# Kernel optimization log

Hardware: AMD Instinct MI355X
Metric: run time of the kernel (lower is better)

The kernel has to match this reference:

```python
import jax, jax.numpy as jnp
import numpy as np

N_NODES = 100000
N_EDGES = 1600000
IN_CH, HID_CH, OUT_CH = 128, 256, 128


def _sage_conv(x, src, dst, W_l, b_l, W_r, n_nodes):
    """PyG SAGEConv with mean aggregation: lin_l(mean_j x_j) + lin_r(x)."""
    # gather source features per edge, scatter-sum into destination nodes
    agg = jax.ops.segment_sum(x[src], dst, num_segments=n_nodes)  # [N, C]
    deg = jax.ops.segment_sum(jnp.ones((src.shape[0],), x.dtype), dst,
                              num_segments=n_nodes)               # [N]
    mean = agg / jnp.maximum(deg, 1.0)[:, None]
    return mean @ W_l + b_l + x @ W_r


def setup_inputs() -> dict:
    key = jax.random.key(0)
    ks = jax.random.split(key, 8)
    x = jax.random.normal(ks[0], (N_NODES, IN_CH), dtype=jnp.float32)
    edge_index = jax.random.randint(ks[1], (2, N_EDGES), 0, N_NODES, dtype=jnp.int64)
    s1 = 1.0 / np.sqrt(IN_CH)
    s2 = 1.0 / np.sqrt(HID_CH)
    W1_l = jax.random.normal(ks[2], (IN_CH, HID_CH), dtype=jnp.float32) * s1
    W1_r = jax.random.normal(ks[3], (IN_CH, HID_CH), dtype=jnp.float32) * s1
    b1 = jnp.zeros((HID_CH,), dtype=jnp.float32)
    W2_l = jax.random.normal(ks[4], (HID_CH, OUT_CH), dtype=jnp.float32) * s2
    W2_r = jax.random.normal(ks[5], (HID_CH, OUT_CH), dtype=jnp.float32) * s2
    b2 = jnp.zeros((OUT_CH,), dtype=jnp.float32)
    return {"x": x, "edge_index": edge_index, "W1_l": W1_l, "b1": b1,
            "W1_r": W1_r, "W2_l": W2_l, "b2": b2, "W2_r": W2_r}


def reference(x, edge_index, W1_l, b1, W1_r, W2_l, b2, W2_r):
    src, dst = edge_index[0], edge_index[1]
    h = _sage_conv(x, src, dst, W1_l, b1, W1_r, N_NODES)
    h = jax.nn.relu(h)
    out = _sage_conv(h, src, dst, W2_l, b2, W2_r, N_NODES)
    return out
```

## Files before the change

kernel.cpp:

```cpp
#include <hip/hip_runtime.h>
#include <cstddef>

#define N_NODES_C 100000
#define N_EDGES_C 1600000

#define NPB 63
#define NB 1588
#define DIV_MAGIC 68174085ULL
#define BCAP 1408
#define SENT_ROW 100000

#define CONV_BLOCKS 12500
#define WB_BLOCKS 512
#define P1_BLOCKS 1563

typedef unsigned short u16;
typedef __attribute__((ext_vector_type(8))) short bf16x8;
typedef __attribute__((ext_vector_type(4))) float f32x4;

__device__ __forceinline__ u16 f2bf(float f) {
    unsigned u = __float_as_uint(f);
    u += 0x7fffu + ((u >> 16) & 1);
    return (u16)(u >> 16);
}
__device__ __forceinline__ float lo16f(unsigned v) {
    return __uint_as_float(v << 16);
}
__device__ __forceinline__ float hi16f(unsigned v) {
    return __uint_as_float(v & 0xffff0000u);
}
__device__ __forceinline__ unsigned bucket_of(int d) {
    return (unsigned)(((unsigned long long)(unsigned)d * DIV_MAGIC) >> 32);
}


__global__ __launch_bounds__(256) void front_fused(
    const float* __restrict__ x, const int* __restrict__ dst,
    const float* __restrict__ W1l, const float* __restrict__ W1r,
    const float* __restrict__ W2l, const float* __restrict__ W2r,
    u16* __restrict__ x_bf, u16* __restrict__ T1l, u16* __restrict__ T1r,
    u16* __restrict__ T2l, u16* __restrict__ T2r,
    int* __restrict__ bucket_counts, u16* __restrict__ p2z) {
    const int b = blockIdx.x;
    const int t = threadIdx.x;
    if (b < CONV_BLOCKS) {
        int i = b * 256 + t;
        if (i < 3200000) {
            float4 v = ((const float4*)x)[i];
            ushort4 o;
            o.x = f2bf(v.x); o.y = f2bf(v.y); o.z = f2bf(v.z); o.w = f2bf(v.w);
            ((ushort4*)x_bf)[i] = o;
        }
    } else if (b < CONV_BLOCKS + WB_BLOCKS) {
        int id = (b - CONV_BLOCKS) * 256 + t;
        int which = id >> 15;
        int r = id & 32767;
        if (which == 0) {
            int n = r >> 7, k = r & 127;
            T1l[r] = f2bf(W1l[k * 256 + n]);
        } else if (which == 1) {
            int n = r >> 7, k = r & 127;
            T1r[r] = f2bf(W1r[k * 256 + n]);
        } else if (which == 2) {
            int n = r >> 8, k = r & 255;
            T2l[r] = f2bf(W2l[k * 128 + n]);
        } else {
            int n = r >> 8, k = r & 255;
            T2r[r] = f2bf(W2r[k * 128 + n]);
        }
    } else if (b < CONV_BLOCKS + WB_BLOCKS + P1_BLOCKS) {
        __shared__ int hist[NB];
        for (int j = t; j < NB; j += 256) hist[j] = 0;
        __syncthreads();
        int i = (b - CONV_BLOCKS - WB_BLOCKS) * 256 + t;
        if (i * 4 < N_EDGES_C) {
            int4 d = ((const int4*)dst)[i];
            atomicAdd(&hist[bucket_of(d.x)], 1);
            atomicAdd(&hist[bucket_of(d.y)], 1);
            atomicAdd(&hist[bucket_of(d.z)], 1);
            atomicAdd(&hist[bucket_of(d.w)], 1);
        }
        __syncthreads();
        for (int j = t; j < NB; j += 256) {
            int c = hist[j];
            if (c) atomicAdd(&bucket_counts[j], c);
        }
    } else {
        uint4 z; z.x = 0; z.y = 0; z.z = 0; z.w = 0;
        if (t < 16)
            ((uint4*)(x_bf + (size_t)SENT_ROW * 128))[t] = z;
        else if (t < 32)
            ((uint4*)(p2z + (size_t)SENT_ROW * 128))[t - 16] = z;
    }
}


__global__ __launch_bounds__(1024) void bucket_scan(const int* __restrict__ counts,
                                                    int* __restrict__ base,
                                                    int* __restrict__ cursor) {
    __shared__ int s[1024];
    int t = threadIdx.x;
    int c0 = counts[2 * t];
    int c1 = counts[2 * t + 1];
    int v = c0 + c1;
    s[t] = v;
    __syncthreads();
    for (int off = 1; off < 1024; off <<= 1) {
        int u = (t >= off) ? s[t - off] : 0;
        __syncthreads();
        s[t] += u;
        __syncthreads();
    }
    int excl = s[t] - v;
    base[2 * t] = excl;
    cursor[2 * t] = excl;
    base[2 * t + 1] = excl + c0;
    cursor[2 * t + 1] = excl + c0;
}


__global__ __launch_bounds__(1024) void p2_scatter(const int* __restrict__ src,
                                                   const int* __restrict__ dst,
                                                   int* __restrict__ cursor,
                                                   unsigned* __restrict__ edge_pkt) {
    __shared__ int hist[NB];
    __shared__ int lbase[NB];
    __shared__ int cur2[NB];
    int t = threadIdx.x;
    for (int j = t; j < NB; j += 1024) { hist[j] = 0; cur2[j] = 0; }
    __syncthreads();

    int4 dd[4];
    int idx[4];
#pragma unroll
    for (int r = 0; r < 4; ++r) {
        int i = blockIdx.x * 4096 + r * 1024 + t;
        idx[r] = i;
        if (i * 4 < N_EDGES_C) {
            int4 d = ((const int4*)dst)[i];
            dd[r] = d;
            atomicAdd(&hist[bucket_of(d.x)], 1);
            atomicAdd(&hist[bucket_of(d.y)], 1);
            atomicAdd(&hist[bucket_of(d.z)], 1);
            atomicAdd(&hist[bucket_of(d.w)], 1);
        }
    }
    __syncthreads();
    for (int j = t; j < NB; j += 1024) {
        int c = hist[j];
        if (c) lbase[j] = atomicAdd(&cursor[j], c);
    }
    __syncthreads();

#pragma unroll
    for (int r = 0; r < 4; ++r) {
        int i = idx[r];
        if (i * 4 < N_EDGES_C) {
            int4 s4 = ((const int4*)src)[i];
            int4 d = dd[r];
            {
                unsigned b = bucket_of(d.x);
                int local = d.x - (int)b * NPB;
                int pos = lbase[b] + atomicAdd(&cur2[b], 1);
                edge_pkt[pos] = ((unsigned)local << 17) | (unsigned)s4.x;
            }
            {
                unsigned b = bucket_of(d.y);
                int local = d.y - (int)b * NPB;
                int pos = lbase[b] + atomicAdd(&cur2[b], 1);
                edge_pkt[pos] = ((unsigned)local << 17) | (unsigned)s4.y;
            }
            {
                unsigned b = bucket_of(d.z);
                int local = d.z - (int)b * NPB;
                int pos = lbase[b] + atomicAdd(&cur2[b], 1);
                edge_pkt[pos] = ((unsigned)local << 17) | (unsigned)s4.z;
            }
            {
                unsigned b = bucket_of(d.w);
                int local = d.w - (int)b * NPB;
                int pos = lbase[b] + atomicAdd(&cur2[b], 1);
                edge_pkt[pos] = ((unsigned)local << 17) | (unsigned)s4.w;
            }
        }
    }
}


template <bool FINAL>
__global__ __launch_bounds__(256, 8) void agg_bucket(const u16* __restrict__ tbl,
                                                     const int* __restrict__ base,
                                                     const unsigned* __restrict__ edge_pkt,
                                                     const u16* __restrict__ resid,
                                                     void* __restrict__ outv) {
    __shared__ unsigned se[BCAP];
    __shared__ int lhist[64];
    __shared__ int lstart[64];
    __shared__ int lcur[64];
    __shared__ int stmp[64];

    const int t = threadIdx.x;
    const int wave = t >> 6;
    const int lane = t & 63;
    const int b = blockIdx.x;

    if (t < 64) lhist[t] = 0;
    __syncthreads();

    const int ebeg = base[b];
    int ecnt = base[b + 1] - ebeg;
    if (ecnt > BCAP) ecnt = BCAP;

    for (int i = t; i < ecnt; i += 256)
        atomicAdd(&lhist[edge_pkt[ebeg + i] >> 17], 1);
    __syncthreads();

    if (t < 64) stmp[t] = lhist[t];
    __syncthreads();
    for (int off = 1; off < 64; off <<= 1) {
        int v = 0;
        if (t < 64 && t >= off) v = stmp[t - off];
        __syncthreads();
        if (t < 64) stmp[t] += v;
        __syncthreads();
    }
    if (t < 64) {
        int excl = stmp[t] - lhist[t];
        lstart[t] = excl;
        lcur[t] = excl;
    }
    __syncthreads();

    for (int i = t; i < ecnt; i += 256) {
        unsigned p = edge_pkt[ebeg + i];
        int pos = atomicAdd(&lcur[p >> 17], 1);
        se[pos] = p & 0x1ffffu;
    }
    __syncthreads();

    const int g = lane >> 4;
    const int li8 = (lane & 15) * 8;

    for (int pass = 0; pass < 4; ++pass) {
        int n = pass * 16 + wave * 4 + g;
        int node = b * NPB + n;
        int d = 0, s0 = 0;
        bool valid = (n < NPB) && (node < N_NODES_C);
        if (valid) { d = lhist[n]; s0 = lstart[n]; }
        int dmax = max(d, __shfl_xor(d, 16, 64));
        dmax = max(dmax, __shfl_xor(dmax, 32, 64));

        float a0 = 0.f, a1 = 0.f, a2 = 0.f, a3 = 0.f;
        float a4 = 0.f, a5 = 0.f, a6 = 0.f, a7 = 0.f;

        for (int j = 0; j < dmax; j += 4) {
            unsigned ix[4];
#pragma unroll
            for (int u = 0; u < 4; ++u) {
                int jj = j + u;
                int sa = s0 + jj;
                if (sa > BCAP - 1) sa = BCAP - 1;
                unsigned sv = se[sa];
                ix[u] = (jj < d) ? sv : (unsigned)SENT_ROW;
            }
            uint4 r0 = *(const uint4*)(tbl + (size_t)ix[0] * 128 + li8);
            uint4 r1 = *(const uint4*)(tbl + (size_t)ix[1] * 128 + li8);
            uint4 r2 = *(const uint4*)(tbl + (size_t)ix[2] * 128 + li8);
            uint4 r3 = *(const uint4*)(tbl + (size_t)ix[3] * 128 + li8);

            a0 += lo16f(r0.x); a1 += hi16f(r0.x);
            a2 += lo16f(r0.y); a3 += hi16f(r0.y);
            a4 += lo16f(r0.z); a5 += hi16f(r0.z);
            a6 += lo16f(r0.w); a7 += hi16f(r0.w);
            a0 += lo16f(r1.x); a1 += hi16f(r1.x);
            a2 += lo16f(r1.y); a3 += hi16f(r1.y);
            a4 += lo16f(r1.z); a5 += hi16f(r1.z);
            a6 += lo16f(r1.w); a7 += hi16f(r1.w);
            a0 += lo16f(r2.x); a1 += hi16f(r2.x);
            a2 += lo16f(r2.y); a3 += hi16f(r2.y);
            a4 += lo16f(r2.z); a5 += hi16f(r2.z);
            a6 += lo16f(r2.w); a7 += hi16f(r2.w);
            a0 += lo16f(r3.x); a1 += hi16f(r3.x);
            a2 += lo16f(r3.y); a3 += hi16f(r3.y);
            a4 += lo16f(r3.z); a5 += hi16f(r3.z);
            a6 += lo16f(r3.w); a7 += hi16f(r3.w);
        }

        if (valid) {
            float inv = d > 0 ? 1.f / (float)d : 0.f;
            if (FINAL) {
                uint4 rp = *(const uint4*)(resid + (size_t)node * 128 + li8);
                float* op = (float*)outv + (size_t)node * 128 + li8;
                float4 o0, o1;
                o0.x = a0 * inv + lo16f(rp.x);
                o0.y = a1 * inv + hi16f(rp.x);
                o0.z = a2 * inv + lo16f(rp.y);
                o0.w = a3 * inv + hi16f(rp.y);
                o1.x = a4 * inv + lo16f(rp.z);
                o1.y = a5 * inv + hi16f(rp.z);
                o1.z = a6 * inv + lo16f(rp.w);
                o1.w = a7 * inv + hi16f(rp.w);
                *(float4*)op = o0;
                *(float4*)(op + 4) = o1;
            } else {
                uint4 o;
                o.x = (unsigned)f2bf(a0 * inv) | ((unsigned)f2bf(a1 * inv) << 16);
                o.y = (unsigned)f2bf(a2 * inv) | ((unsigned)f2bf(a3 * inv) << 16);
                o.z = (unsigned)f2bf(a4 * inv) | ((unsigned)f2bf(a5 * inv) << 16);
                o.w = (unsigned)f2bf(a6 * inv) | ((unsigned)f2bf(a7 * inv) << 16);
                *(uint4*)((u16*)outv + (size_t)node * 128 + li8) = o;
            }
        }
    }
}


__global__ __launch_bounds__(256) void fused_l1l2(
    const u16* __restrict__ A1 , const u16* __restrict__ A2 ,
    const u16* __restrict__ T1l, const u16* __restrict__ T1r,
    const u16* __restrict__ T2l, const u16* __restrict__ T2r,
    const float* __restrict__ b1, const float* __restrict__ b2,
    u16* __restrict__ p2, u16* __restrict__ outp, int M) {
    alignas(16) __shared__ u16 hfrag[64 * 256];
    alignas(16) __shared__ u16 As[64 * 32];
    alignas(16) __shared__ u16 Bs[256 * 32];

    const int tid = threadIdx.x;
    const int lane = tid & 63;
    const int wave = tid >> 6;
    const int qm = lane & 15;
    const int quad = lane >> 4;
    const int m0 = blockIdx.x * 64;

    const int wr0 = (wave >> 1) * 32;
    const int wc0 = (wave & 1) * 128;
    f32x4 acch[2][8];
#pragma unroll
    for (int i = 0; i < 2; ++i)
#pragma unroll
        for (int j = 0; j < 8; ++j) acch[i][j] = (f32x4){0.f, 0.f, 0.f, 0.f};

#pragma unroll
    for (int mat = 0; mat < 2; ++mat) {
        const u16* __restrict__ A = mat ? A2 : A1;
        const u16* __restrict__ W = mat ? T1r : T1l;
#pragma unroll
        for (int k0 = 0; k0 < 128; k0 += 32) {
            {
                int c = tid;
                int row = c >> 2, kc = c & 3;
                __builtin_amdgcn_global_load_lds(
                    (const __attribute__((address_space(1))) unsigned*)(
                        A + (size_t)(m0 + row) * 128 + k0 + kc * 8),
                    (__attribute__((address_space(3))) unsigned*)(As + c * 8), 16, 0, 0);
            }
#pragma unroll
            for (int r = 0; r < 4; ++r) {
                int c = r * 256 + tid;
                int row = c >> 2, kc = c & 3;
                __builtin_amdgcn_global_load_lds(
                    (const __attribute__((address_space(1))) unsigned*)(
                        W + (size_t)row * 128 + k0 + kc * 8),
                    (__attribute__((address_space(3))) unsigned*)(Bs + c * 8), 16, 0, 0);
            }
            __syncthreads();
            bf16x8 af[2], bf[8];
#pragma unroll
            for (int i = 0; i < 2; ++i)
                af[i] = *(const bf16x8*)(As + (wr0 + i * 16 + qm) * 32 + quad * 8);
#pragma unroll
            for (int j = 0; j < 8; ++j)
                bf[j] = *(const bf16x8*)(Bs + (wc0 + j * 16 + qm) * 32 + quad * 8);
#pragma unroll
            for (int i = 0; i < 2; ++i)
#pragma unroll
                for (int j = 0; j < 8; ++j)
                    acch[i][j] = __builtin_amdgcn_mfma_f32_16x16x32_bf16(
                        af[i], bf[j], acch[i][j], 0, 0, 0);
            __syncthreads();
        }
    }

#pragma unroll
    for (int j = 0; j < 8; ++j) {
        int n = wc0 + j * 16 + qm;
        float bb = b1[n];
        int ks = n >> 5, quadB = (n >> 3) & 3, jB = n & 7;
#pragma unroll
        for (int i = 0; i < 2; ++i) {
#pragma unroll
            for (int r = 0; r < 4; ++r) {
                int mloc = wr0 + i * 16 + quad * 4 + r;
                float v = fmaxf(acch[i][j][r] + bb, 0.f);
                hfrag[((ks * 4 + (mloc >> 4)) * 16 + (mloc & 15)) * 32 + quadB * 8 + jB] =
                    f2bf(v);
            }
        }
    }
    __syncthreads();

    const int wrB = (wave >> 1) * 32;
    const int wcB = (wave & 1) * 64;
    f32x4 accp[2][4], acco[2][4];
#pragma unroll
    for (int i = 0; i < 2; ++i)
#pragma unroll
        for (int j = 0; j < 4; ++j) {
            accp[i][j] = (f32x4){0.f, 0.f, 0.f, 0.f};
            acco[i][j] = (f32x4){0.f, 0.f, 0.f, 0.f};
        }

#pragma unroll
    for (int ks = 0; ks < 8; ++ks) {
#pragma unroll
        for (int r = 0; r < 4; ++r) {
            int c = r * 256 + tid;
            int matc = c >> 9;
            int row = (c >> 2) & 127;
            int kc = c & 3;
            const u16* W = matc ? T2r : T2l;
            __builtin_amdgcn_global_load_lds(
                (const __attribute__((address_space(1))) unsigned*)(
                    W + (size_t)row * 256 + ks * 32 + kc * 8),
                (__attribute__((address_space(3))) unsigned*)(Bs + c * 8), 16, 0, 0);
        }
        __syncthreads();
        bf16x8 af[2], bfl[4], bfr[4];
#pragma unroll
        for (int i = 0; i < 2; ++i)
            af[i] = *(const bf16x8*)(hfrag +
                                     ((ks * 4 + (wrB >> 4) + i) * 16 + qm) * 32 + quad * 8);
#pragma unroll
        for (int j = 0; j < 4; ++j) {
            bfl[j] = *(const bf16x8*)(Bs + (wcB + j * 16 + qm) * 32 + quad * 8);
            bfr[j] = *(const bf16x8*)(Bs + 4096 + (wcB + j * 16 + qm) * 32 + quad * 8);
        }
#pragma unroll
        for (int i = 0; i < 2; ++i)
#pragma unroll
            for (int j = 0; j < 4; ++j) {
                accp[i][j] = __builtin_amdgcn_mfma_f32_16x16x32_bf16(af[i], bfl[j],
                                                                    accp[i][j], 0, 0, 0);
                acco[i][j] = __builtin_amdgcn_mfma_f32_16x16x32_bf16(af[i], bfr[j],
                                                                    acco[i][j], 0, 0, 0);
            }
        __syncthreads();
    }

#pragma unroll
    for (int j = 0; j < 4; ++j) {
        int n = wcB + j * 16 + qm;
        float bb2 = b2[n];
#pragma unroll
        for (int i = 0; i < 2; ++i) {
#pragma unroll
            for (int r = 0; r < 4; ++r) {
                int row = m0 + wrB + i * 16 + quad * 4 + r;
                if (row < M) {
                    p2[(size_t)row * 128 + n] = f2bf(accp[i][j][r]);
                    outp[(size_t)row * 128 + n] = f2bf(acco[i][j][r] + bb2);
                }
            }
        }
    }
}


extern "C" void kernel_launch(void* const* d_in, const int* in_sizes, int n_in,
                              void* d_out, int out_size, void* d_ws, size_t ws_size,
                              hipStream_t stream) {
    const float* x = (const float*)d_in[0];
    const int* ei = (const int*)d_in[1];
    const float* W1l = (const float*)d_in[2];
    const float* b1 = (const float*)d_in[3];
    const float* W1r = (const float*)d_in[4];
    const float* W2l = (const float*)d_in[5];
    const float* b2 = (const float*)d_in[6];
    const float* W2r = (const float*)d_in[7];
    float* out = (float*)d_out;

    const int* src = ei;
    const int* dst = ei + N_EDGES_C;

    int* iw = (int*)d_ws;
    int* bucket_counts = iw;
    int* bucket_base = iw + 2048;
    int* cursor = iw + 4096;
    unsigned* edge_pkt = (unsigned*)(iw + 6144);
    u16* T1l = (u16*)(iw + 1606144);
    u16* T1r = T1l + 32768;
    u16* T2l = T1r + 32768;
    u16* T2r = T2l + 32768;
    u16* ub = (u16*)((char*)d_ws + (8u << 20));
    u16* x_bf = ub;
    u16* mean1 = ub + 12850000;
    u16* p2 = ub + 25700000;
    u16* outp = ub + 38550000;

    hipMemsetAsync(bucket_counts, 0, 2048 * sizeof(int), stream);

    front_fused<<<CONV_BLOCKS + WB_BLOCKS + P1_BLOCKS + 1, 256, 0, stream>>>(
        x, dst, W1l, W1r, W2l, W2r, x_bf, T1l, T1r, T2l, T2r, bucket_counts, p2);
    bucket_scan<<<1, 1024, 0, stream>>>(bucket_counts, bucket_base, cursor);
    p2_scatter<<<(N_EDGES_C / 4 + 4095) / 4096, 1024, 0, stream>>>(src, dst, cursor,
                                                                   edge_pkt);

    agg_bucket<false><<<NB, 256, 0, stream>>>(x_bf, bucket_base, edge_pkt, nullptr,
                                              mean1);
    fused_l1l2<<<(N_NODES_C + 63) / 64, 256, 0, stream>>>(
        mean1, x_bf, T1l, T1r, T2l, T2r, b1, b2, p2, outp, N_NODES_C);
    agg_bucket<true><<<NB, 256, 0, stream>>>(p2, bucket_base, edge_pkt, outp, out);
}
```

Before: 401.9 us.

## Fuse layer-1 aggregation into GEMM kernel with 64-node power-of-two buckets

```diff
diff --git a/kernel.cpp b/kernel.cpp
--- a/kernel.cpp
+++ b/kernel.cpp
@@ -4,9 +4,8 @@
 #define N_NODES_C 100000
 #define N_EDGES_C 1600000
 
-#define NPB 63
-#define NB 1588
-#define DIV_MAGIC 68174085ULL
+#define NPB 64
+#define NB 1563
 #define BCAP 1408
 #define SENT_ROW 100000
 
@@ -28,9 +27,6 @@
 }
 __device__ __forceinline__ float hi16f(unsigned v) {
     return __uint_as_float(v & 0xffff0000u);
-}
-__device__ __forceinline__ unsigned bucket_of(int d) {
-    return (unsigned)(((unsigned long long)(unsigned)d * DIV_MAGIC) >> 32);
 }
 
 
@@ -75,10 +71,10 @@
         int i = (b - CONV_BLOCKS - WB_BLOCKS) * 256 + t;
         if (i * 4 < N_EDGES_C) {
             int4 d = ((const int4*)dst)[i];
-            atomicAdd(&hist[bucket_of(d.x)], 1);
-            atomicAdd(&hist[bucket_of(d.y)], 1);
-            atomicAdd(&hist[bucket_of(d.z)], 1);
-            atomicAdd(&hist[bucket_of(d.w)], 1);
+            atomicAdd(&hist[d.x >> 6], 1);
+            atomicAdd(&hist[d.y >> 6], 1);
+            atomicAdd(&hist[d.z >> 6], 1);
+            atomicAdd(&hist[d.w >> 6], 1);
         }
         __syncthreads();
         for (int j = t; j < NB; j += 256) {
@@ -139,10 +135,10 @@
         if (i * 4 < N_EDGES_C) {
             int4 d = ((const int4*)dst)[i];
             dd[r] = d;
-            atomicAdd(&hist[bucket_of(d.x)], 1);
-            atomicAdd(&hist[bucket_of(d.y)], 1);
-            atomicAdd(&hist[bucket_of(d.z)], 1);
-            atomicAdd(&hist[bucket_of(d.w)], 1);
+            atomicAdd(&hist[d.x >> 6], 1);
+            atomicAdd(&hist[d.y >> 6], 1);
+            atomicAdd(&hist[d.z >> 6], 1);
+            atomicAdd(&hist[d.w >> 6], 1);
         }
     }
     __syncthreads();
@@ -159,27 +155,23 @@
             int4 s4 = ((const int4*)src)[i];
             int4 d = dd[r];
             {
-                unsigned b = bucket_of(d.x);
-                int local = d.x - (int)b * NPB;
-                int pos = lbase[b] + atomicAdd(&cur2[b], 1);
+                int bk = d.x >> 6, local = d.x & 63;
+                int pos = lbase[bk] + atomicAdd(&cur2[bk], 1);
                 edge_pkt[pos] = ((unsigned)local << 17) | (unsigned)s4.x;
             }
             {
-                unsigned b = bucket_of(d.y);
-                int local = d.y - (int)b * NPB;
-                int pos = lbase[b] + atomicAdd(&cur2[b], 1);
+                int bk = d.y >> 6, local = d.y & 63;
+                int pos = lbase[bk] + atomicAdd(&cur2[bk], 1);
                 edge_pkt[pos] = ((unsigned)local << 17) | (unsigned)s4.y;
             }
             {
-                unsigned b = bucket_of(d.z);
-                int local = d.z - (int)b * NPB;
-                int pos = lbase[b] + atomicAdd(&cur2[b], 1);
+                int bk = d.z >> 6, local = d.z & 63;
+                int pos = lbase[bk] + atomicAdd(&cur2[bk], 1);
                 edge_pkt[pos] = ((unsigned)local << 17) | (unsigned)s4.z;
             }
             {
-                unsigned b = bucket_of(d.w);
-                int local = d.w - (int)b * NPB;
-                int pos = lbase[b] + atomicAdd(&cur2[b], 1);
+                int bk = d.w >> 6, local = d.w & 63;
+                int pos = lbase[bk] + atomicAdd(&cur2[bk], 1);
                 edge_pkt[pos] = ((unsigned)local << 17) | (unsigned)s4.w;
             }
         }
@@ -187,66 +179,85 @@
 }
 
 
-template <bool FINAL>
-__global__ __launch_bounds__(256, 8) void agg_bucket(const u16* __restrict__ tbl,
-                                                     const int* __restrict__ base,
-                                                     const unsigned* __restrict__ edge_pkt,
-                                                     const u16* __restrict__ resid,
-                                                     void* __restrict__ outv) {
+__global__ __launch_bounds__(256, 2) void fused_gemm_agg(
+    const u16* __restrict__ x_bf,
+    const int* __restrict__ base, const unsigned* __restrict__ edge_pkt,
+    const u16* __restrict__ T1l, const u16* __restrict__ T1r,
+    const u16* __restrict__ T2l, const u16* __restrict__ T2r,
+    const float* __restrict__ b1, const float* __restrict__ b2,
+    u16* __restrict__ p2, u16* __restrict__ outp, int M) {
+    alignas(16) __shared__ u16 uni[64 * 256];
+    alignas(16) __shared__ u16 Bs[8192];
     __shared__ unsigned se[BCAP];
     __shared__ int lhist[64];
     __shared__ int lstart[64];
     __shared__ int lcur[64];
     __shared__ int stmp[64];
 
-    const int t = threadIdx.x;
-    const int wave = t >> 6;
-    const int lane = t & 63;
+    u16* const meanS = uni;
+    u16* const xS = uni + 64 * 128;
+    u16* const hfrag = uni;
+
+    const int tid = threadIdx.x;
+    const int lane = tid & 63;
+    const int wave = tid >> 6;
+    const int qm = lane & 15;
+    const int quad = lane >> 4;
     const int b = blockIdx.x;
-
-    if (t < 64) lhist[t] = 0;
+    const int m0 = b * 64;
+
+#pragma unroll
+    for (int r = 0; r < 4; ++r) {
+        int c = r * 256 + tid;
+        int row = c >> 4, q16 = c & 15;
+        __builtin_amdgcn_global_load_lds(
+            (const __attribute__((address_space(1))) unsigned*)(
+                x_bf + (size_t)(m0 + row) * 128 + ((q16 ^ (row & 7)) * 8)),
+            (__attribute__((address_space(3))) unsigned*)(xS + c * 8), 16, 0, 0);
+    }
+
+    if (tid < 64) lhist[tid] = 0;
     __syncthreads();
 
     const int ebeg = base[b];
     int ecnt = base[b + 1] - ebeg;
     if (ecnt > BCAP) ecnt = BCAP;
 
-    for (int i = t; i < ecnt; i += 256)
+    for (int i = tid; i < ecnt; i += 256)
         atomicAdd(&lhist[edge_pkt[ebeg + i] >> 17], 1);
     __syncthreads();
 
-    if (t < 64) stmp[t] = lhist[t];
+    if (tid < 64) stmp[tid] = lhist[tid];
     __syncthreads();
     for (int off = 1; off < 64; off <<= 1) {
         int v = 0;
-        if (t < 64 && t >= off) v = stmp[t - off];
-        __syncthreads();
-        if (t < 64) stmp[t] += v;
-        __syncthreads();
-    }
-    if (t < 64) {
-        int excl = stmp[t] - lhist[t];
-        lstart[t] = excl;
-        lcur[t] = excl;
-    }
-    __syncthreads();
-
-    for (int i = t; i < ecnt; i += 256) {
+        if (tid < 64 && tid >= off) v = stmp[tid - off];
+        __syncthreads();
+        if (tid < 64) stmp[tid] += v;
+        __syncthreads();
+    }
+    if (tid < 64) {
+        int excl = stmp[tid] - lhist[tid];
+        lstart[tid] = excl;
+        lcur[tid] = excl;
+    }
+    __syncthreads();
+
+    for (int i = tid; i < ecnt; i += 256) {
         unsigned p = edge_pkt[ebeg + i];
         int pos = atomicAdd(&lcur[p >> 17], 1);
         se[pos] = p & 0x1ffffu;
     }
     __syncthreads();
 
-    const int g = lane >> 4;
-    const int li8 = (lane & 15) * 8;
+    const int g = quad;
+    const int li16 = qm;
+    const int li8 = li16 * 8;
 
     for (int pass = 0; pass < 4; ++pass) {
         int n = pass * 16 + wave * 4 + g;
-        int node = b * NPB + n;
-        int d = 0, s0 = 0;
-        bool valid = (n < NPB) && (node < N_NODES_C);
-        if (valid) { d = lhist[n]; s0 = lstart[n]; }
+        int d = lhist[n];
+        int s0 = lstart[n];
         int dmax = max(d, __shfl_xor(d, 16, 64));
         dmax = max(dmax, __shfl_xor(dmax, 32, 64));
 
@@ -263,10 +274,10 @@
                 unsigned sv = se[sa];
                 ix[u] = (jj < d) ? sv : (unsigned)SENT_ROW;
             }
-            uint4 r0 = *(const uint4*)(tbl + (size_t)ix[0] * 128 + li8);
-            uint4 r1 = *(const uint4*)(tbl + (size_t)ix[1] * 128 + li8);
-            uint4 r2 = *(const uint4*)(tbl + (size_t)ix[2] * 128 + li8);
-            uint4 r3 = *(const uint4*)(tbl + (size_t)ix[3] * 128 + li8);
+            uint4 r0 = *(const uint4*)(x_bf + (size_t)ix[0] * 128 + li8);
+            uint4 r1 = *(const uint4*)(x_bf + (size_t)ix[1] * 128 + li8);
+            uint4 r2 = *(const uint4*)(x_bf + (size_t)ix[2] * 128 + li8);
+            uint4 r3 = *(const uint4*)(x_bf + (size_t)ix[3] * 128 + li8);
 
             a0 += lo16f(r0.x); a1 += hi16f(r0.x);
             a2 += lo16f(r0.y); a3 += hi16f(r0.y);
@@ -286,51 +297,15 @@
             a6 += lo16f(r3.w); a7 += hi16f(r3.w);
         }
 
-        if (valid) {
-            float inv = d > 0 ? 1.f / (float)d : 0.f;
-            if (FINAL) {
-                uint4 rp = *(const uint4*)(resid + (size_t)node * 128 + li8);
-                float* op = (float*)outv + (size_t)node * 128 + li8;
-                float4 o0, o1;
-                o0.x = a0 * inv + lo16f(rp.x);
-                o0.y = a1 * inv + hi16f(rp.x);
-                o0.z = a2 * inv + lo16f(rp.y);
-                o0.w = a3 * inv + hi16f(rp.y);
-                o1.x = a4 * inv + lo16f(rp.z);
-                o1.y = a5 * inv + hi16f(rp.z);
-                o1.z = a6 * inv + lo16f(rp.w);
-                o1.w = a7 * inv + hi16f(rp.w);
-                *(float4*)op = o0;
-                *(float4*)(op + 4) = o1;
-            } else {
-                uint4 o;
-                o.x = (unsigned)f2bf(a0 * inv) | ((unsigned)f2bf(a1 * inv) << 16);
-                o.y = (unsigned)f2bf(a2 * inv) | ((unsigned)f2bf(a3 * inv) << 16);
-                o.z = (unsigned)f2bf(a4 * inv) | ((unsigned)f2bf(a5 * inv) << 16);
-                o.w = (unsigned)f2bf(a6 * inv) | ((unsigned)f2bf(a7 * inv) << 16);
-                *(uint4*)((u16*)outv + (size_t)node * 128 + li8) = o;
-            }
-        }
-    }
-}
-
-
-__global__ __launch_bounds__(256) void fused_l1l2(
-    const u16* __restrict__ A1 , const u16* __restrict__ A2 ,
-    const u16* __restrict__ T1l, const u16* __restrict__ T1r,
-    const u16* __restrict__ T2l, const u16* __restrict__ T2r,
-    const float* __restrict__ b1, const float* __restrict__ b2,
-    u16* __restrict__ p2, u16* __restrict__ outp, int M) {
-    alignas(16) __shared__ u16 hfrag[64 * 256];
-    alignas(16) __shared__ u16 As[64 * 32];
-    alignas(16) __shared__ u16 Bs[256 * 32];
-
-    const int tid = threadIdx.x;
-    const int lane = tid & 63;
-    const int wave = tid >> 6;
-    const int qm = lane & 15;
-    const int quad = lane >> 4;
-    const int m0 = blockIdx.x * 64;
+        float inv = d > 0 ? 1.f / (float)d : 0.f;
+        uint4 o;
+        o.x = (unsigned)f2bf(a0 * inv) | ((unsigned)f2bf(a1 * inv) << 16);
+        o.y = (unsigned)f2bf(a2 * inv) | ((unsigned)f2bf(a3 * inv) << 16);
+        o.z = (unsigned)f2bf(a4 * inv) | ((unsigned)f2bf(a5 * inv) << 16);
+        o.w = (unsigned)f2bf(a6 * inv) | ((unsigned)f2bf(a7 * inv) << 16);
+        *(uint4*)(meanS + n * 128 + ((li16 ^ (n & 7)) * 8)) = o;
+    }
+    __syncthreads();
 
     const int wr0 = (wave >> 1) * 32;
     const int wc0 = (wave & 1) * 128;
@@ -342,41 +317,39 @@
 
 #pragma unroll
     for (int mat = 0; mat < 2; ++mat) {
-        const u16* __restrict__ A = mat ? A2 : A1;
         const u16* __restrict__ W = mat ? T1r : T1l;
+        const u16* Al = mat ? xS : meanS;
 #pragma unroll
         for (int k0 = 0; k0 < 128; k0 += 32) {
-            {
-                int c = tid;
-                int row = c >> 2, kc = c & 3;
-                __builtin_amdgcn_global_load_lds(
-                    (const __attribute__((address_space(1))) unsigned*)(
-                        A + (size_t)(m0 + row) * 128 + k0 + kc * 8),
-                    (__attribute__((address_space(3))) unsigned*)(As + c * 8), 16, 0, 0);
-            }
 #pragma unroll
             for (int r = 0; r < 4; ++r) {
                 int c = r * 256 + tid;
                 int row = c >> 2, kc = c & 3;
                 __builtin_amdgcn_global_load_lds(
                     (const __attribute__((address_space(1))) unsigned*)(
-                        W + (size_t)row * 128 + k0 + kc * 8),
+                        W + (size_t)row * 128 + k0 + ((kc ^ (row & 3)) * 8)),
                     (__attribute__((address_space(3))) unsigned*)(Bs + c * 8), 16, 0, 0);
             }
             __syncthreads();
-            bf16x8 af[2], bf[8];
-#pragma unroll
-            for (int i = 0; i < 2; ++i)
-                af[i] = *(const bf16x8*)(As + (wr0 + i * 16 + qm) * 32 + quad * 8);
-#pragma unroll
-            for (int j = 0; j < 8; ++j)
-                bf[j] = *(const bf16x8*)(Bs + (wc0 + j * 16 + qm) * 32 + quad * 8);
+            int ch0 = k0 >> 3;
+            bf16x8 af[2], bfv[8];
+#pragma unroll
+            for (int i = 0; i < 2; ++i) {
+                int row = wr0 + i * 16 + qm;
+                af[i] = *(const bf16x8*)(Al + row * 128 +
+                                         (((ch0 + quad) ^ (row & 7)) * 8));
+            }
+#pragma unroll
+            for (int j = 0; j < 8; ++j) {
+                int rB = wc0 + j * 16 + qm;
+                bfv[j] = *(const bf16x8*)(Bs + rB * 32 + ((quad ^ (rB & 3)) * 8));
+            }
 #pragma unroll
             for (int i = 0; i < 2; ++i)
 #pragma unroll
                 for (int j = 0; j < 8; ++j)
                     acch[i][j] = __builtin_amdgcn_mfma_f32_16x16x32_bf16(
-                        af[i], bf[j], acch[i][j], 0, 0, 0);
+                        af[i], bfv[j], acch[i][j], 0, 0, 0);
             __syncthreads();
         }
     }
@@ -421,7 +394,7 @@
             const u16* W = matc ? T2r : T2l;
             __builtin_amdgcn_global_load_lds(
                 (const __attribute__((address_space(1))) unsigned*)(
-                    W + (size_t)row * 256 + ks * 32 + kc * 8),
+                    W + (size_t)row * 256 + ks * 32 + ((kc ^ (row & 3)) * 8)),
                 (__attribute__((address_space(3))) unsigned*)(Bs + c * 8), 16, 0, 0);
         }
         __syncthreads();
@@ -432,8 +405,9 @@
                                      ((ks * 4 + (wrB >> 4) + i) * 16 + qm) * 32 + quad * 8);
 #pragma unroll
         for (int j = 0; j < 4; ++j) {
-            bfl[j] = *(const bf16x8*)(Bs + (wcB + j * 16 + qm) * 32 + quad * 8);
-            bfr[j] = *(const bf16x8*)(Bs + 4096 + (wcB + j * 16 + qm) * 32 + quad * 8);
+            int rB = wcB + j * 16 + qm;
+            bfl[j] = *(const bf16x8*)(Bs + rB * 32 + ((quad ^ (rB & 3)) * 8));
+            bfr[j] = *(const bf16x8*)(Bs + 4096 + rB * 32 + ((quad ^ (rB & 3)) * 8));
         }
 #pragma unroll
         for (int i = 0; i < 2; ++i)
@@ -461,6 +435,124 @@
                     outp[(size_t)row * 128 + n] = f2bf(acco[i][j][r] + bb2);
                 }
             }
+        }
+    }
+}
+
+
+__global__ __launch_bounds__(256, 8) void agg_final(const u16* __restrict__ tbl,
+                                                    const int* __restrict__ base,
+                                                    const unsigned* __restrict__ edge_pkt,
+                                                    const u16* __restrict__ resid,
+                                                    float* __restrict__ outv) {
+    __shared__ unsigned se[BCAP];
+    __shared__ int lhist[64];
+    __shared__ int lstart[64];
+    __shared__ int lcur[64];
+    __shared__ int stmp[64];
+
+    const int t = threadIdx.x;
+    const int wave = t >> 6;
+    const int lane = t & 63;
+    const int b = blockIdx.x;
+
+    if (t < 64) lhist[t] = 0;
+    __syncthreads();
+
+    const int ebeg = base[b];
+    int ecnt = base[b + 1] - ebeg;
+    if (ecnt > BCAP) ecnt = BCAP;
+
+    for (int i = t; i < ecnt; i += 256)
+        atomicAdd(&lhist[edge_pkt[ebeg + i] >> 17], 1);
+    __syncthreads();
+
+    if (t < 64) stmp[t] = lhist[t];
+    __syncthreads();
+    for (int off = 1; off < 64; off <<= 1) {
+        int v = 0;
+        if (t < 64 && t >= off) v = stmp[t - off];
+        __syncthreads();
+        if (t < 64) stmp[t] += v;
+        __syncthreads();
+    }
+    if (t < 64) {
+        int excl = stmp[t] - lhist[t];
+        lstart[t] = excl;
+        lcur[t] = excl;
+    }
+    __syncthreads();
+
+    for (int i = t; i < ecnt; i += 256) {
+        unsigned p = edge_pkt[ebeg + i];
+        int pos = atomicAdd(&lcur[p >> 17], 1);
+        se[pos] = p & 0x1ffffu;
+    }
+    __syncthreads();
+
+    const int g = lane >> 4;
+    const int li8 = (lane & 15) * 8;
+
+    for (int pass = 0; pass < 4; ++pass) {
+        int n = pass * 16 + wave * 4 + g;
+        int node = b * NPB + n;
+        bool valid = node < N_NODES_C;
+        int d = 0, s0 = 0;
+        if (valid) { d = lhist[n]; s0 = lstart[n]; }
+        int dmax = max(d, __shfl_xor(d, 16, 64));
+        dmax = max(dmax, __shfl_xor(dmax, 32, 64));
+
+        float a0 = 0.f, a1 = 0.f, a2 = 0.f, a3 = 0.f;
+        float a4 = 0.f, a5 = 0.f, a6 = 0.f, a7 = 0.f;
+
+        for (int j = 0; j < dmax; j += 4) {
+            unsigned ix[4];
+#pragma unroll
+            for (int u = 0; u < 4; ++u) {
+                int jj = j + u;
+                int sa = s0 + jj;
+                if (sa > BCAP - 1) sa = BCAP - 1;
+                unsigned sv = se[sa];
+                ix[u] = (jj < d) ? sv : (unsigned)SENT_ROW;
+            }
+            uint4 r0 = *(const uint4*)(tbl + (size_t)ix[0] * 128 + li8);
+            uint4 r1 = *(const uint4*)(tbl + (size_t)ix[1] * 128 + li8);
+            uint4 r2 = *(const uint4*)(tbl + (size_t)ix[2] * 128 + li8);
+            uint4 r3 = *(const uint4*)(tbl + (size_t)ix[3] * 128 + li8);
+
+            a0 += lo16f(r0.x); a1 += hi16f(r0.x);
+            a2 += lo16f(r0.y); a3 += hi16f(r0.y);
+            a4 += lo16f(r0.z); a5 += hi16f(r0.z);
+            a6 += lo16f(r0.w); a7 += hi16f(r0.w);
+            a0 += lo16f(r1.x); a1 += hi16f(r1.x);
+            a2 += lo16f(r1.y); a3 += hi16f(r1.y);
+            a4 += lo16f(r1.z); a5 += hi16f(r1.z);
+            a6 += lo16f(r1.w); a7 += hi16f(r1.w);
+            a0 += lo16f(r2.x); a1 += hi16f(r2.x);
+            a2 += lo16f(r2.y); a3 += hi16f(r2.y);
+            a4 += lo16f(r2.z); a5 += hi16f(r2.z);
+            a6 += lo16f(r2.w); a7 += hi16f(r2.w);
+            a0 += lo16f(r3.x); a1 += hi16f(r3.x);
+            a2 += lo16f(r3.y); a3 += hi16f(r3.y);
+            a4 += lo16f(r3.z); a5 += hi16f(r3.z);
+            a6 += lo16f(r3.w); a7 += hi16f(r3.w);
+        }
+
+        if (valid) {
+            float inv = d > 0 ? 1.f / (float)d : 0.f;
+            uint4 rp = *(const uint4*)(resid + (size_t)node * 128 + li8);
+            float* op = outv + (size_t)node * 128 + li8;
+            float4 o0, o1;
+            o0.x = a0 * inv + lo16f(rp.x);
+            o0.y = a1 * inv + hi16f(rp.x);
+            o0.z = a2 * inv + lo16f(rp.y);
+            o0.w = a3 * inv + hi16f(rp.y);
+            o1.x = a4 * inv + lo16f(rp.z);
+            o1.y = a5 * inv + hi16f(rp.z);
+            o1.z = a6 * inv + lo16f(rp.w);
+            o1.w = a7 * inv + hi16f(rp.w);
+            *(float4*)op = o0;
+            *(float4*)(op + 4) = o1;
         }
     }
 }
@@ -493,9 +585,8 @@
     u16* T2r = T2l + 32768;
     u16* ub = (u16*)((char*)d_ws + (8u << 20));
     u16* x_bf = ub;
-    u16* mean1 = ub + 12850000;
-    u16* p2 = ub + 25700000;
-    u16* outp = ub + 38550000;
+    u16* p2 = ub + 12850000;
+    u16* outp = ub + 25700000;
 
     hipMemsetAsync(bucket_counts, 0, 2048 * sizeof(int), stream);
 
@@ -505,9 +596,7 @@
     p2_scatter<<<(N_EDGES_C / 4 + 4095) / 4096, 1024, 0, stream>>>(src, dst, cursor,
                                                                    edge_pkt);
 
-    agg_bucket<false><<<NB, 256, 0, stream>>>(x_bf, bucket_base, edge_pkt, nullptr,
-                                              mean1);
-    fused_l1l2<<<(N_NODES_C + 63) / 64, 256, 0, stream>>>(
-        mean1, x_bf, T1l, T1r, T2l, T2r, b1, b2, p2, outp, N_NODES_C);
-    agg_bucket<true><<<NB, 256, 0, stream>>>(p2, bucket_base, edge_pkt, outp, out);
-}
+    fused_gemm_agg<<<NB, 256, 0, stream>>>(x_bf, bucket_base, edge_pkt, T1l, T1r,
+                                           T2l, T2r, b1, b2, p2, outp, N_NODES_C);
+    agg_final<<<NB, 256, 0, stream>>>(p2, bucket_base, edge_pkt, outp, out);
+}
```

New measurement: 396.9 us. No clear change (-1.2%).
